# Kernel tuning notes

Hardware: AMD Instinct MI355X
Metric: run time of the kernel (lower is better)

Reference implementation:

```python
import jax, jax.numpy as jnp
import numpy as np
from jax import lax

AR_VOCAB = 25
EN_VOCAB = 25
N_CLASSES = 1 + AR_VOCAB + EN_VOCAB + AR_VOCAB * EN_VOCAB  # full_table id layout
NEG = -jnp.inf
BIG_NEG = -1e30  # acts as log(0) in float32 (exp underflows to exactly 0) but keeps grads finite
T_LEN = 256
V_LEN = 256


def setup_inputs() -> dict:
    key = jax.random.key(0)
    k1, k2 = jax.random.split(key)
    ar_sent = jax.random.randint(k1, (1, T_LEN), 0, AR_VOCAB)
    en_sent = jax.random.randint(k2, (1, V_LEN), 0, EN_VOCAB)
    # self.weights = log(uniform) over target classes
    weights = jnp.full((N_CLASSES,), -jnp.log(jnp.float32(N_CLASSES)), dtype=jnp.float32)
    return {"ar_sent": ar_sent, "en_sent": en_sent, "weights": weights}


def _chain(c, m):
    """Solve a[0]=c[0]; a[i]=logaddexp(c[i], m[i]+a[i-1]) in parallel.
    a[i] = s[i] + logcumsumexp(c - s)[i] with s = prefix sums of m (s[0]=0)."""
    s = jnp.concatenate([jnp.zeros((1,), c.dtype), jnp.cumsum(m[1:])])
    return s + lax.associative_scan(jnp.logaddexp, c - s)


def _safe_lse(x, axis):
    """Stable logsumexp that returns -inf (with zero gradient) on empty/-inf slices."""
    m = lax.stop_gradient(jnp.max(x, axis=axis, keepdims=True))
    m = jnp.where(jnp.isfinite(m), m, 0.0)
    s = jnp.sum(jnp.exp(x - m), axis=axis)
    ok = s > 0
    return jnp.squeeze(m, axis=axis) + jnp.where(ok, jnp.log(jnp.where(ok, s, 1.0)), NEG)


def _forward(ar, en, weights):
    # ar: [T] int, en: [V] int, weights: [C] log-probs
    T, V = ar.shape[0], en.shape[0]
    del_ids = 1 + ar                                               # [T]
    ins_ids = 1 + AR_VOCAB + en                                    # [V]
    sub_ids = 1 + AR_VOCAB + EN_VOCAB + EN_VOCAB * ar[:, None] + en[None, :]  # [T,V]
    w_del = weights[del_ids]   # [T]
    w_ins = weights[ins_ids]   # [V]
    w_sub = weights[sub_ids]   # [T,V]

    # ---- alpha DP (forward lattice) ----
    # row 0: alpha[0,0]=0, alpha[0,v]=alpha[0,v-1]+w_ins[v]
    c0 = jnp.full((V,), BIG_NEG, weights.dtype).at[0].set(0.0)
    row0 = _chain(c0, w_ins)

    def fstep(prev, xs):
        wd, ws = xs  # w_del[t] scalar, w_sub[t,:] [V]
        # c[v] = logaddexp(w_del[t]+alpha[t-1,v], w_sub[t,v]+alpha[t-1,v-1]); v=0 has no sub term
        c = jnp.concatenate([(wd + prev[0])[None],
                             jnp.logaddexp(wd + prev[1:], ws[1:] + prev[:-1])])
        row = _chain(c, w_ins)  # adds within-row insertion recurrence
        return row, row

    _, frows = lax.scan(fstep, row0, (w_del[1:], w_sub[1:]))
    alpha = jnp.concatenate([row0[None], frows], axis=0)  # [T,V]

    # ---- beta DP (backward lattice) ----
    m_rev = w_ins[::-1]
    cT = jnp.full((V,), BIG_NEG, weights.dtype).at[-1].set(0.0)
    rowT = _chain(cT[::-1], m_rev)[::-1]

    def bstep(nxt, xs):
        wd, ws = xs
        # c[v] = logaddexp(w_del[t]+beta[t+1,v], w_sub[t,v]+beta[t+1,v+1]); v=V-1 has no sub term
        c = jnp.concatenate([jnp.logaddexp(wd + nxt[:-1], ws[:-1] + nxt[1:]),
                             (wd + nxt[-1])[None]])
        row = _chain(c[::-1], m_rev)[::-1]  # beta[t,v] += w_ins[v]+beta[t,v+1] recurrence
        return row, row

    _, brows = lax.scan(bstep, rowT, (w_del[:-1], w_sub[:-1]), reverse=True)
    beta = jnp.concatenate([brows, rowT[None]], axis=0)  # [T,V]

    # ---- expected edit-operation counts (log space) ----
    cls = jnp.arange(N_CLASSES)
    w = weights[None, None, :]
    md = jnp.where(del_ids[1:, None, None] == cls, 0.0, NEG)   # [T-1,1,C] one-hot log mask
    mi = jnp.where(ins_ids[None, 1:, None] == cls, 0.0, NEG)   # [1,V-1,C]
    ms = jnp.where(sub_ids[1:, 1:, None] == cls, 0.0, NEG)     # [T-1,V-1,C]
    ed = alpha[:-1, :, None] + w + md + beta[1:, :, None]      # expected deletions
    ei = alpha[:, :-1, None] + w + mi + beta[:, 1:, None]      # expected insertions
    es = alpha[:-1, :-1, None] + w + ms + beta[1:, 1:, None]   # expected substitutions
    return _safe_lse(jnp.stack([_safe_lse(ed, (0, 1)),
                                _safe_lse(ei, (0, 1)),
                                _safe_lse(es, (0, 1))]), 0)    # [C]


def reference(ar_sent, en_sent, weights):
    return _forward(ar_sent[0], en_sent[0], weights)
```

## Files before the change

### kernel.cpp

```cpp
#include <hip/hip_runtime.h>
#include <math.h>

#define NCLS 676
#define NEG_SENTINEL -3.0e38f
#define LN2F 0.6931471805599453f
#define JPAD 768
#define RS 256
#define QIP_OFF 692
#define WSE_OFF (QIP_OFF + JPAD)
#define SHM_FLOATS (WSE_OFF + 25 * JPAD + 32)
#define MAGIC 0x13579BDFu

__device__ __forceinline__ float dpp_shr1(float x) {
  return __int_as_float(
      __builtin_amdgcn_update_dpp(0, __float_as_int(x), 0x138, 0xF, 0xF, false));
}
__device__ __forceinline__ float dpp_shl1(float x) {
  return __int_as_float(
      __builtin_amdgcn_update_dpp(0, __float_as_int(x), 0x130, 0xF, 0xF, false));
}
__device__ __forceinline__ int dpp_shr1_i(int x) {
  return __builtin_amdgcn_update_dpp(0, x, 0x138, 0xF, 0xF, false);
}
__device__ __forceinline__ int dpp_shl1_i(int x) {
  return __builtin_amdgcn_update_dpp(0, x, 0x130, 0xF, 0xF, false);
}
__device__ __forceinline__ float pow2c(int d) {
  d = min(max(d, -126), 126);
  return __int_as_float((d + 127) << 23);
}

__global__ __launch_bounds__(256, 1) void k_fused(const int* __restrict__ ar,
                                                  const int* __restrict__ en,
                                                  const float* __restrict__ wts,
                                                  float* __restrict__ aD,
                                                  float* __restrict__ bD,
                                                  int* __restrict__ aEb,
                                                  int* __restrict__ bEb,
                                                  float* __restrict__ S,
                                                  unsigned* __restrict__ flags,
                                                  float* __restrict__ out) {
  const int tid = threadIdx.x;
  __shared__ alignas(16) float shm[SHM_FLOATS];

  if (blockIdx.x >= 2) {
    float* bins = shm;
    int* ctl = (int*)(shm + 680);
    for (int c = tid; c < NCLS; c += 256) bins[c] = 0.f;
    if (tid == 0) ctl[0] = 0;
    __syncthreads();
    if (tid == 0) {
      while (__hip_atomic_load(&flags[0], __ATOMIC_RELAXED,
                               __HIP_MEMORY_SCOPE_AGENT) != MAGIC ||
             __hip_atomic_load(&flags[1], __ATOMIC_RELAXED,
                               __HIP_MEMORY_SCOPE_AGENT) != MAGIC)
        __builtin_amdgcn_s_sleep(16);
      (void)__hip_atomic_load(&flags[0], __ATOMIC_ACQUIRE,
                              __HIP_MEMORY_SCOPE_AGENT);
      __hip_atomic_store(&ctl[0], 1, __ATOMIC_RELEASE,
                         __HIP_MEMORY_SCOPE_WORKGROUP);
    } else if (tid >= 64) {
      float x = 1.0f + (float)tid;
      while (__hip_atomic_load(&ctl[0], __ATOMIC_RELAXED,
                               __HIP_MEMORY_SCOPE_WORKGROUP) == 0) {
#pragma unroll
        for (int z = 0; z < 128; ++z) x = fmaf(x, 1.0000001f, 1.0e-7f);
      }
      if (x == 123.456f) atomicAdd(&S[0], 0.f);
    }
    __syncthreads();
    const float M = __logf(aD[510 * RS]) +
                    (float)aEb[63 * 64 + 63] * LN2F + 16.0f;
    const int j = tid;
    const int e = en[j];
#pragma unroll
    for (int u = 0; u < 4; ++u) {
      const int d = ((int)blockIdx.x - 2) * 4 + u;
      if (d <= 510) {
        const int i = d - j;
        if (i >= 0 && i <= 255) {
          const float bM = bD[d * RS + 255 - i];
          if (bM > 0.f) {
            const int bEx =
                (d == 510) ? 0 : bEb[((509 - d) >> 3) * 64 + (i >> 2)];
            const float lb = __logf(bM) + (float)bEx * LN2F - M;
            const int a = ar[i];
            if (i >= 1) {
              float aM = aD[(d - 1) * RS + 256 - i];
              if (aM > 0.f) {
                int eA =
                    (d == 1) ? 0 : aEb[((d - 2) >> 3) * 64 + ((i - 1) >> 2)];
                float L = __logf(aM) + (float)eA * LN2F + lb;
                atomicAdd(&bins[1 + a], __expf(fminf(L, 0.f)));
              }
            }
            if (j >= 1) {
              float aM = aD[(d - 1) * RS + 255 - i];
              if (aM > 0.f) {
                int eA = (d == 1) ? 0 : aEb[((d - 2) >> 3) * 64 + (i >> 2)];
                float L = __logf(aM) + (float)eA * LN2F + lb;
                atomicAdd(&bins[26 + e], __expf(fminf(L, 0.f)));
              }
              if (i >= 1) {
                float aM2 = aD[(d - 2) * RS + 256 - i];
                if (aM2 > 0.f) {
                  int eA2 =
                      (d == 2) ? 0 : aEb[((d - 3) >> 3) * 64 + ((i - 1) >> 2)];
                  float L2 = __logf(aM2) + (float)eA2 * LN2F + lb;
                  atomicAdd(&bins[51 + 25 * a + e], __expf(fminf(L2, 0.f)));
                }
              }
            }
          }
        }
      }
    }
    __syncthreads();
    for (int c = tid; c < NCLS; c += 256)
      if (bins[c] != 0.f) atomicAdd(&S[c], bins[c]);
    __syncthreads();
    if (tid == 0) {
      unsigned n = __hip_atomic_fetch_add(&flags[2], 1u, __ATOMIC_ACQ_REL,
                                          __HIP_MEMORY_SCOPE_AGENT);
      ctl[1] = ((n & 127u) == 127u);
    }
    __syncthreads();
    if (ctl[1]) {
      for (int c = tid; c < NCLS; c += 256) {
        float s = __hip_atomic_load(&S[c], __ATOMIC_RELAXED,
                                    __HIP_MEMORY_SCOPE_AGENT);
        out[c] = (c != 0 && s > 0.f) ? (wts[c] + M + __logf(s)) : NEG_SENTINEL;
      }
    }
    return;
  }

  float* pw = shm;
  float* qip = shm + QIP_OFF;
  float* wsE = shm + WSE_OFF;
  for (int c = tid; c < NCLS; c += 256) pw[c] = __expf(wts[c]);
  {
    float4* z = (float4*)(shm + NCLS);
    const int nz = (SHM_FLOATS - NCLS) / 4;
    for (int t = tid; t < nz; t += 256) z[t] = make_float4(0.f, 0.f, 0.f, 0.f);
  }
  if (blockIdx.x == 0) {
    for (int c = tid; c < NCLS; c += 256) S[c] = 0.f;
    if (tid == 0)
      __hip_atomic_store(&flags[2], 0u, __ATOMIC_RELAXED,
                         __HIP_MEMORY_SCOPE_AGENT);
  }
  __syncthreads();
  {
    int j = tid;
    int ee = en[j];
    qip[255 + j] = pw[26 + ee];
#pragma unroll
    for (int a = 0; a < 25; ++a) wsE[a * JPAD + 255 + j] = pw[51 + 25 * a + ee];
  }
  __syncthreads();
  if (tid >= 64) return;
  const int lane = tid;

  const int i0 = 4 * lane;
  float wdl[4];
  const float* rowp[4];
#pragma unroll
  for (int k = 0; k < 4; ++k) {
    int a = ar[i0 + k];
    wdl[k] = pw[1 + a];
    rowp[k] = wsE + a * JPAD;
  }
  float P1[4] = {0.f, 0.f, 0.f, 0.f};
  float P2[4] = {0.f, 0.f, 0.f, 0.f};
  int e1 = 0;

  if (blockIdx.x == 0) {
    if (lane == 0) { P1[0] = 1.f; aD[255] = 1.f; }
    int e0 = 252 - i0;
    float* sp = aD + RS + 252 - i0;
    int* ep = aEb + lane;
    float W[4][12], Q[12];

#define LOAD_A(EB, W, Q)                                                   \
  {                                                                        \
    _Pragma("unroll") for (int k = 0; k < 4; ++k) {                        \
      const float4* p = (const float4*)(rowp[k] + (EB));                   \
      float4 va = p[0], vb = p[1], vc = p[2];                              \
      W[k][0] = va.x; W[k][1] = va.y; W[k][2] = va.z; W[k][3] = va.w;      \
      W[k][4] = vb.x; W[k][5] = vb.y; W[k][6] = vb.z; W[k][7] = vb.w;      \
      W[k][8] = vc.x; W[k][9] = vc.y; W[k][10] = vc.z; W[k][11] = vc.w;    \
    }                                                                      \
    const float4* q = (const float4*)(qip + (EB));                         \
    float4 qa = q[0], qb = q[1], qc = q[2];                                \
    Q[0] = qa.x; Q[1] = qa.y; Q[2] = qa.z; Q[3] = qa.w;                    \
    Q[4] = qb.x; Q[5] = qb.y; Q[6] = qb.z; Q[7] = qb.w;                    \
    Q[8] = qc.x; Q[9] = qc.y; Q[10] = qc.z; Q[11] = qc.w;                  \
  }

    LOAD_A(e0, W, Q);
    for (int pr = 0; pr < 64; ++pr) {
      *ep = e1; ep += 64;
      int t1e = dpp_shr1_i(e1);
      float f1n = pow2c(t1e - e1);
      float pmc = dpp_shr1(P2[3]) * f1n;
#pragma unroll
      for (int u = 0; u < 8; ++u) {
        float pm1 = dpp_shr1(P1[3]) * f1n;
        float pm2 = pmc;
        float cu[4];
#pragma unroll
        for (int k = 0; k < 4; ++k) {
          float a1 = (k == 0) ? pm1 : P1[k - 1];
          float a2 = (k == 0) ? pm2 : P2[k - 1];
          cu[k] = fmaf(wdl[k], a1,
                       fmaf(W[k][4 + u - k], a2, Q[4 + u - k] * P1[k]));
        }
        *(float4*)sp = make_float4(cu[3], cu[2], cu[1], cu[0]);
        sp += RS;
#pragma unroll
        for (int k = 0; k < 4; ++k) {
          P2[k] = P1[k]; P1[k] = cu[k];
        }
        pmc = pm1;
      }
      e0 += 8;
      LOAD_A(e0, W, Q);
      float m = fmaxf(fmaxf(P1[0], P1[1]), fmaxf(P1[2], P1[3]));
      int ex = (m > 0.f) ? ((__float_as_int(m) >> 23) - 126) : (t1e - e1);
      float sc = pow2c(-ex);
#pragma unroll
      for (int k = 0; k < 4; ++k) {
        P1[k] *= sc; P2[k] *= sc;
      }
      e1 += ex;
    }
  } else {
    if (lane == 63) P1[3] = 1.f;
    if (lane == 0) bD[510 * RS] = 1.f;
    int e0 = 764 - i0;
    float* sp = bD + 509 * RS + 252 - i0;
    int* ep = bEb + lane;
    float W[4][16], Q[16];

#define LOAD_B(EB, W, Q)                                                   \
  {                                                                        \
    _Pragma("unroll") for (int k = 0; k < 4; ++k) {                        \
      const float4* p = (const float4*)(rowp[k] + (EB));                   \
      float4 va = p[0], vb = p[1], vc = p[2], vd = p[3];                   \
      W[k][0] = va.x; W[k][1] = va.y; W[k][2] = va.z; W[k][3] = va.w;      \
      W[k][4] = vb.x; W[k][5] = vb.y; W[k][6] = vb.z; W[k][7] = vb.w;      \
      W[k][8] = vc.x; W[k][9] = vc.y; W[k][10] = vc.z; W[k][11] = vc.w;    \
      W[k][12] = vd.x; W[k][13] = vd.y; W[k][14] = vd.z; W[k][15] = vd.w;  \
    }                                                                      \
    const float4* q = (const float4*)(qip + (EB));                         \
    float4 qa = q[0], qb = q[1], qc = q[2], qd = q[3];                     \
    Q[0] = qa.x; Q[1] = qa.y; Q[2] = qa.z; Q[3] = qa.w;                    \
    Q[4] = qb.x; Q[5] = qb.y; Q[6] = qb.z; Q[7] = qb.w;                    \
    Q[8] = qc.x; Q[9] = qc.y; Q[10] = qc.z; Q[11] = qc.w;                  \
    Q[12] = qd.x; Q[13] = qd.y; Q[14] = qd.z; Q[15] = qd.w;                \
  }

    LOAD_B(e0, W, Q);
    for (int pr = 0; pr < 64; ++pr) {
      *ep = e1; ep += 64;
      int t1e = dpp_shl1_i(e1);
      float f1n = pow2c(t1e - e1);
      float pmc = dpp_shl1(P2[0]) * f1n;
#pragma unroll
      for (int u = 0; u < 8; ++u) {
        float pm1 = dpp_shl1(P1[0]) * f1n;
        float pm2 = pmc;
        float cu[4];
#pragma unroll
        for (int k = 0; k < 4; ++k) {
          float a1 = (k == 3) ? pm1 : P1[k + 1];
          float a2 = (k == 3) ? pm2 : P2[k + 1];
          cu[k] = fmaf(wdl[k], a1,
                       fmaf(W[k][12 - u - k], a2, Q[13 - u - k] * P1[k]));
        }
        *(float4*)sp = make_float4(cu[3], cu[2], cu[1], cu[0]);
        sp -= RS;
#pragma unroll
        for (int k = 0; k < 4; ++k) {
          P2[k] = P1[k]; P1[k] = cu[k];
        }
        pmc = pm1;
      }
      e0 -= 8;
      LOAD_B(e0, W, Q);
      float m = fmaxf(fmaxf(P1[0], P1[1]), fmaxf(P1[2], P1[3]));
      int ex = (m > 0.f) ? ((__float_as_int(m) >> 23) - 126) : (t1e - e1);
      float sc = pow2c(-ex);
#pragma unroll
      for (int k = 0; k < 4; ++k) {
        P1[k] *= sc; P2[k] *= sc;
      }
      e1 += ex;
    }
  }

  __threadfence();
  if (lane == 0)
    __hip_atomic_store(&flags[blockIdx.x], MAGIC, __ATOMIC_RELEASE,
                       __HIP_MEMORY_SCOPE_AGENT);
}

extern "C" void kernel_launch(void* const* d_in, const int* in_sizes, int n_in,
                              void* d_out, int out_size, void* d_ws, size_t ws_size,
                              hipStream_t stream) {
  const int* ar = (const int*)d_in[0];
  const int* en = (const int*)d_in[1];
  const float* wts = (const float*)d_in[2];
  float* aD = (float*)d_ws;
  float* bDraw = aD + 514 * RS;
  float* bD = bDraw + 2 * RS;
  int* aEb = (int*)(bDraw + 514 * RS);
  int* bEb = aEb + 4096;
  float* S = (float*)(bEb + 4096);
  unsigned* flags = (unsigned*)(S + NCLS);
  k_fused<<<130, 256, 0, stream>>>(ar, en, wts, aD, bD, aEb, bEb, S, flags,
                                   (float*)d_out);
}
```

Before: 96.04 us.

## Split fused DP kernel into separate DP and reduction kernels with sliced accumulators

Moves the expected-count reduction out of the persistent fused kernel into a second launch, so the 128 reduction blocks no longer wait on spin flags, and only start after the DP kernel has finished. Global accumulators are spread over 8 slices to reduce atomic contention, and the last block sums the slices. The leftover wait code in k_dp still spins in blocks 2..129 and no longer does useful work. This adds a kernel launch boundary in exchange.

Result: slower. 97.97 us (+2.0%).

```diff
diff --git a/kernel.cpp b/kernel.cpp
--- a/kernel.cpp
+++ b/kernel.cpp
@@ -10,6 +10,7 @@
 #define WSE_OFF (QIP_OFF + JPAD)
 #define SHM_FLOATS (WSE_OFF + 25 * JPAD + 32)
 #define MAGIC 0x13579BDFu
+#define NSLICE 8
 
 __device__ __forceinline__ float dpp_shr1(float x) {
   return __int_as_float(
@@ -30,23 +31,20 @@
   return __int_as_float((d + 127) << 23);
 }
 
-__global__ __launch_bounds__(256, 1) void k_fused(const int* __restrict__ ar,
-                                                  const int* __restrict__ en,
-                                                  const float* __restrict__ wts,
-                                                  float* __restrict__ aD,
-                                                  float* __restrict__ bD,
-                                                  int* __restrict__ aEb,
-                                                  int* __restrict__ bEb,
-                                                  float* __restrict__ S,
-                                                  unsigned* __restrict__ flags,
-                                                  float* __restrict__ out) {
+__global__ __launch_bounds__(256, 1) void k_dp(const int* __restrict__ ar,
+                                               const int* __restrict__ en,
+                                               const float* __restrict__ wts,
+                                               float* __restrict__ aD,
+                                               float* __restrict__ bD,
+                                               int* __restrict__ aEb,
+                                               int* __restrict__ bEb,
+                                               float* __restrict__ S,
+                                               unsigned* __restrict__ flags) {
   const int tid = threadIdx.x;
   __shared__ alignas(16) float shm[SHM_FLOATS];
 
   if (blockIdx.x >= 2) {
-    float* bins = shm;
-    int* ctl = (int*)(shm + 680);
-    for (int c = tid; c < NCLS; c += 256) bins[c] = 0.f;
+    int* ctl = (int*)shm;
     if (tid == 0) ctl[0] = 0;
     __syncthreads();
     if (tid == 0) {
@@ -55,8 +53,6 @@
              __hip_atomic_load(&flags[1], __ATOMIC_RELAXED,
                                __HIP_MEMORY_SCOPE_AGENT) != MAGIC)
         __builtin_amdgcn_s_sleep(16);
-      (void)__hip_atomic_load(&flags[0], __ATOMIC_ACQUIRE,
-                              __HIP_MEMORY_SCOPE_AGENT);
       __hip_atomic_store(&ctl[0], 1, __ATOMIC_RELEASE,
                          __HIP_MEMORY_SCOPE_WORKGROUP);
     } else if (tid >= 64) {
@@ -67,70 +63,6 @@
         for (int z = 0; z < 128; ++z) x = fmaf(x, 1.0000001f, 1.0e-7f);
       }
       if (x == 123.456f) atomicAdd(&S[0], 0.f);
-    }
-    __syncthreads();
-    const float M = __logf(aD[510 * RS]) +
-                    (float)aEb[63 * 64 + 63] * LN2F + 16.0f;
-    const int j = tid;
-    const int e = en[j];
-#pragma unroll
-    for (int u = 0; u < 4; ++u) {
-      const int d = ((int)blockIdx.x - 2) * 4 + u;
-      if (d <= 510) {
-        const int i = d - j;
-        if (i >= 0 && i <= 255) {
-          const float bM = bD[d * RS + 255 - i];
-          if (bM > 0.f) {
-            const int bEx =
-                (d == 510) ? 0 : bEb[((509 - d) >> 3) * 64 + (i >> 2)];
-            const float lb = __logf(bM) + (float)bEx * LN2F - M;
-            const int a = ar[i];
-            if (i >= 1) {
-              float aM = aD[(d - 1) * RS + 256 - i];
-              if (aM > 0.f) {
-                int eA =
-                    (d == 1) ? 0 : aEb[((d - 2) >> 3) * 64 + ((i - 1) >> 2)];
-                float L = __logf(aM) + (float)eA * LN2F + lb;
-                atomicAdd(&bins[1 + a], __expf(fminf(L, 0.f)));
-              }
-            }
-            if (j >= 1) {
-              float aM = aD[(d - 1) * RS + 255 - i];
-              if (aM > 0.f) {
-                int eA = (d == 1) ? 0 : aEb[((d - 2) >> 3) * 64 + (i >> 2)];
-                float L = __logf(aM) + (float)eA * LN2F + lb;
-                atomicAdd(&bins[26 + e], __expf(fminf(L, 0.f)));
-              }
-              if (i >= 1) {
-                float aM2 = aD[(d - 2) * RS + 256 - i];
-                if (aM2 > 0.f) {
-                  int eA2 =
-                      (d == 2) ? 0 : aEb[((d - 3) >> 3) * 64 + ((i - 1) >> 2)];
-                  float L2 = __logf(aM2) + (float)eA2 * LN2F + lb;
-                  atomicAdd(&bins[51 + 25 * a + e], __expf(fminf(L2, 0.f)));
-                }
-              }
-            }
-          }
-        }
-      }
-    }
-    __syncthreads();
-    for (int c = tid; c < NCLS; c += 256)
-      if (bins[c] != 0.f) atomicAdd(&S[c], bins[c]);
-    __syncthreads();
-    if (tid == 0) {
-      unsigned n = __hip_atomic_fetch_add(&flags[2], 1u, __ATOMIC_ACQ_REL,
-                                          __HIP_MEMORY_SCOPE_AGENT);
-      ctl[1] = ((n & 127u) == 127u);
-    }
-    __syncthreads();
-    if (ctl[1]) {
-      for (int c = tid; c < NCLS; c += 256) {
-        float s = __hip_atomic_load(&S[c], __ATOMIC_RELAXED,
-                                    __HIP_MEMORY_SCOPE_AGENT);
-        out[c] = (c != 0 && s > 0.f) ? (wts[c] + M + __logf(s)) : NEG_SENTINEL;
-      }
     }
     return;
   }
@@ -145,7 +77,7 @@
     for (int t = tid; t < nz; t += 256) z[t] = make_float4(0.f, 0.f, 0.f, 0.f);
   }
   if (blockIdx.x == 0) {
-    for (int c = tid; c < NCLS; c += 256) S[c] = 0.f;
+    for (int c = tid; c < NSLICE * NCLS; c += 256) S[c] = 0.f;
     if (tid == 0)
       __hip_atomic_store(&flags[2], 0u, __ATOMIC_RELAXED,
                          __HIP_MEMORY_SCOPE_AGENT);
@@ -306,6 +238,89 @@
                        __HIP_MEMORY_SCOPE_AGENT);
 }
 
+__global__ __launch_bounds__(256) void k_red(const int* __restrict__ ar,
+                                             const int* __restrict__ en,
+                                             const float* __restrict__ wts,
+                                             const float* __restrict__ aD,
+                                             const float* __restrict__ bD,
+                                             const int* __restrict__ aEb,
+                                             const int* __restrict__ bEb,
+                                             float* __restrict__ S,
+                                             unsigned* __restrict__ flags,
+                                             float* __restrict__ out) {
+  const int tid = threadIdx.x;
+  __shared__ float bins[NCLS];
+  __shared__ int ctl;
+  for (int c = tid; c < NCLS; c += 256) bins[c] = 0.f;
+  __syncthreads();
+  const float M = __logf(aD[510 * RS]) +
+                  (float)aEb[63 * 64 + 63] * LN2F + 16.0f;
+  const int j = tid;
+  const int e = en[j];
+#pragma unroll
+  for (int u = 0; u < 4; ++u) {
+    const int d = (int)blockIdx.x * 4 + u;
+    if (d <= 510) {
+      const int i = d - j;
+      if (i >= 0 && i <= 255) {
+        const float bM = bD[d * RS + 255 - i];
+        if (bM > 0.f) {
+          const int bEx =
+              (d == 510) ? 0 : bEb[((509 - d) >> 3) * 64 + (i >> 2)];
+          const float lb = __logf(bM) + (float)bEx * LN2F - M;
+          const int a = ar[i];
+          if (i >= 1) {
+            float aM = aD[(d - 1) * RS + 256 - i];
+            if (aM > 0.f) {
+              int eA = (d == 1) ? 0 : aEb[((d - 2) >> 3) * 64 + ((i - 1) >> 2)];
+              float L = __logf(aM) + (float)eA * LN2F + lb;
+              atomicAdd(&bins[1 + a], __expf(fminf(L, 0.f)));
+            }
+          }
+          if (j >= 1) {
+            float aM = aD[(d - 1) * RS + 255 - i];
+            if (aM > 0.f) {
+              int eA = (d == 1) ? 0 : aEb[((d - 2) >> 3) * 64 + (i >> 2)];
+              float L = __logf(aM) + (float)eA * LN2F + lb;
+              atomicAdd(&bins[26 + e], __expf(fminf(L, 0.f)));
+            }
+            if (i >= 1) {
+              float aM2 = aD[(d - 2) * RS + 256 - i];
+              if (aM2 > 0.f) {
+                int eA2 =
+                    (d == 2) ? 0 : aEb[((d - 3) >> 3) * 64 + ((i - 1) >> 2)];
+                float L2 = __logf(aM2) + (float)eA2 * LN2F + lb;
+                atomicAdd(&bins[51 + 25 * a + e], __expf(fminf(L2, 0.f)));
+              }
+            }
+          }
+        }
+      }
+    }
+  }
+  __syncthreads();
+  float* Ss = S + (blockIdx.x & (NSLICE - 1)) * NCLS;
+  for (int c = tid; c < NCLS; c += 256)
+    if (bins[c] != 0.f) atomicAdd(&Ss[c], bins[c]);
+  __syncthreads();
+  if (tid == 0) {
+    unsigned n = __hip_atomic_fetch_add(&flags[2], 1u, __ATOMIC_ACQ_REL,
+                                        __HIP_MEMORY_SCOPE_AGENT);
+    ctl = ((n & 127u) == 127u);
+  }
+  __syncthreads();
+  if (ctl) {
+    for (int c = tid; c < NCLS; c += 256) {
+      float s = 0.f;
+#pragma unroll
+      for (int q = 0; q < NSLICE; ++q)
+        s += __hip_atomic_load(&S[q * NCLS + c], __ATOMIC_RELAXED,
+                               __HIP_MEMORY_SCOPE_AGENT);
+      out[c] = (c != 0 && s > 0.f) ? (wts[c] + M + __logf(s)) : NEG_SENTINEL;
+    }
+  }
+}
+
 extern "C" void kernel_launch(void* const* d_in, const int* in_sizes, int n_in,
                               void* d_out, int out_size, void* d_ws, size_t ws_size,
                               hipStream_t stream) {
@@ -318,7 +333,8 @@
   int* aEb = (int*)(bDraw + 514 * RS);
   int* bEb = aEb + 4096;
   float* S = (float*)(bEb + 4096);
-  unsigned* flags = (unsigned*)(S + NCLS);
-  k_fused<<<130, 256, 0, stream>>>(ar, en, wts, aD, bD, aEb, bEb, S, flags,
-                                   (float*)d_out);
-}
+  unsigned* flags = (unsigned*)(S + NSLICE * NCLS);
+  k_dp<<<130, 256, 0, stream>>>(ar, en, wts, aD, bD, aEb, bEb, S, flags);
+  k_red<<<128, 256, 0, stream>>>(ar, en, wts, aD, bD, aEb, bEb, S, flags,
+                                 (float*)d_out);
+}
```
